# Kernel optimization log

Hardware: AMD Instinct MI355X
Metric: run time of the kernel (lower is better)

The kernel has to match this reference:

```python
import jax, jax.numpy as jnp
import numpy as np

D_MODEL = 1024
N_HEADS = 16
D_HEAD = D_MODEL // N_HEADS


def setup_inputs() -> dict:
    key = jax.random.key(0)
    ks = jax.random.split(key, 11)
    s = 0.02
    return {
        "X": jax.random.normal(ks[0], (4, 2048, D_MODEL), dtype=jnp.float32),
        "ln_gamma": jnp.ones((D_MODEL,), jnp.float32),
        "ln_beta": jnp.zeros((D_MODEL,), jnp.float32),
        "Wq": jax.random.normal(ks[1], (D_MODEL, D_MODEL), jnp.float32) * s,
        "bq": jnp.zeros((D_MODEL,), jnp.float32),
        "Wk": jax.random.normal(ks[2], (D_MODEL, D_MODEL), jnp.float32) * s,
        "bk": jnp.zeros((D_MODEL,), jnp.float32),
        "Wv": jax.random.normal(ks[3], (D_MODEL, D_MODEL), jnp.float32) * s,
        "bv": jnp.zeros((D_MODEL,), jnp.float32),
        "Wo": jax.random.normal(ks[4], (D_MODEL, D_MODEL), jnp.float32) * s,
        "bo": jnp.zeros((D_MODEL,), jnp.float32),
    }


def _attention(X, ln_gamma, ln_beta, Wq, bq, Wk, bk, Wv, bv, Wo, bo):
    B, S, D = X.shape
    H, Dh = N_HEADS, D_HEAD
    # LayerNorm over last dim
    mu = jnp.mean(X, axis=-1, keepdims=True)
    var = jnp.mean(jnp.square(X - mu), axis=-1, keepdims=True)
    Xn = (X - mu) * jax.lax.rsqrt(var + 1e-5) * ln_gamma + ln_beta
    # Projections (torch Linear: x @ W.T + b; W is [out, in])
    Q = (Xn @ Wq.T + bq).reshape(B, S, H, Dh).transpose(0, 2, 1, 3)
    K = (Xn @ Wk.T + bk).reshape(B, S, H, Dh).transpose(0, 2, 1, 3)
    V = (Xn @ Wv.T + bv).reshape(B, S, H, Dh).transpose(0, 2, 1, 3)
    scale = 1.0 / np.sqrt(Dh).astype(np.float32)
    scores = jnp.einsum("bhqd,bhkd->bhqk", Q * scale, K)  # [B,H,S,S]
    # p_dropout = 0.0 -> dropout is identity (applied before mask in original)
    # additive causal mask: 0 where q >= k, -inf otherwise
    causal = jnp.tril(jnp.ones((S, S), jnp.bool_))
    scores = jnp.where(causal, scores, -jnp.inf)
    A = jax.nn.softmax(scores, axis=-1)
    AV = jnp.einsum("bhqk,bhkd->bhqd", A, V)
    merged = AV.transpose(0, 2, 1, 3).reshape(B, S, D)
    return merged @ Wo.T + bo


def reference(X, ln_gamma, ln_beta, Wq, bq, Wk, bk, Wv, bv, Wo, bo):
    return _attention(X, ln_gamma, ln_beta, Wq, bq, Wk, bk, Wv, bv, Wo, bo)
```

## Files before the change

kernel.cpp:

```cpp
#include <hip/hip_runtime.h>

#define D_MODEL 1024
#define N_HEADS 16
#define D_HEAD 64
#define BATCH 4
#define SEQ 2048
#define TOKENS (BATCH * SEQ)
#define D_QKV 3072

#define QBLK 64
#define KBLK 64

typedef __attribute__((ext_vector_type(8))) short short8;
typedef __attribute__((ext_vector_type(4))) float f32x4;

__device__ __forceinline__ unsigned short f2bf(float f) {
    unsigned u = __float_as_uint(f);
    u += 0x7fffu + ((u >> 16) & 1u);
    return (unsigned short)(u >> 16);
}
__device__ __forceinline__ void gload16(const unsigned short* g, unsigned short* lds) {
    __builtin_amdgcn_global_load_lds((const __attribute__((address_space(1))) void*)g,
                                     (__attribute__((address_space(3))) void*)lds, 16, 0, 0);
}

__global__ void ln_kernel(const float* __restrict__ X, const float* __restrict__ gamma,
                          const float* __restrict__ beta, unsigned short* __restrict__ Xn) {
    const int t = blockIdx.x;
    const int tid = threadIdx.x;
    const float4 v = ((const float4*)(X + (size_t)t * D_MODEL))[tid];
    float s  = v.x + v.y + v.z + v.w;
    float s2 = v.x * v.x + v.y * v.y + v.z * v.z + v.w * v.w;
    for (int off = 32; off > 0; off >>= 1) {
        s  += __shfl_xor(s,  off);
        s2 += __shfl_xor(s2, off);
    }
    __shared__ float sh[8];
    const int wv = tid >> 6;
    if ((tid & 63) == 0) { sh[wv] = s; sh[4 + wv] = s2; }
    __syncthreads();
    const float ts  = sh[0] + sh[1] + sh[2] + sh[3];
    const float ts2 = sh[4] + sh[5] + sh[6] + sh[7];
    const float mu  = ts * (1.0f / D_MODEL);
    const float var = ts2 * (1.0f / D_MODEL) - mu * mu;
    const float rs  = rsqrtf(var + 1e-5f);
    const float4 gm = ((const float4*)gamma)[tid];
    const float4 bt = ((const float4*)beta)[tid];
    ushort4 o;
    o.x = f2bf((v.x - mu) * rs * gm.x + bt.x);
    o.y = f2bf((v.y - mu) * rs * gm.y + bt.y);
    o.z = f2bf((v.z - mu) * rs * gm.z + bt.z);
    o.w = f2bf((v.w - mu) * rs * gm.w + bt.w);
    ((ushort4*)Xn)[(size_t)t * (D_MODEL / 4) + tid] = o;
}

__global__ void cvt_all(const float* __restrict__ Wq, const float* __restrict__ Wk,
                        const float* __restrict__ Wv, const float* __restrict__ Wo,
                        unsigned short* __restrict__ Wqkv, unsigned short* __restrict__ WoB) {
    const int i = blockIdx.x * blockDim.x + threadIdx.x;
    const int mtx  = i >> 18;
    const int elem = i & 262143;
    const float* src;
    unsigned short* dst;
    if (mtx == 0)      { src = Wq; dst = Wqkv; }
    else if (mtx == 1) { src = Wk; dst = Wqkv + (1 << 20); }
    else if (mtx == 2) { src = Wv; dst = Wqkv + (2 << 20); }
    else               { src = Wo; dst = WoB; }
    const float4 v = ((const float4*)src)[elem];
    ushort4 o;
    o.x = f2bf(v.x); o.y = f2bf(v.y); o.z = f2bf(v.z); o.w = f2bf(v.w);
    ((ushort4*)dst)[elem] = o;
}

__global__ void transpose_v(const unsigned short* __restrict__ QKV, unsigned short* __restrict__ out) {
    __shared__ __attribute__((aligned(16))) unsigned short T[64][72];
    const int tid = threadIdx.x;
    const int s0 = blockIdx.x * 64;
    const int n0 = blockIdx.y * 64;
    const int b  = blockIdx.z;
    const int r = tid >> 2, c = (tid & 3) * 16;
    const unsigned short* ip = QKV + ((size_t)(b * SEQ + s0 + r)) * D_QKV + 2048 + n0 + c;
    *(short8*)&T[r][c]     = *(const short8*)ip;
    *(short8*)&T[r][c + 8] = *(const short8*)(ip + 8);
    __syncthreads();
    unsigned short* op = out + ((size_t)(b * D_MODEL + n0 + r)) * SEQ + s0 + c;
    short8 o0, o1;
    #pragma unroll
    for (int j = 0; j < 8; ++j) { o0[j] = (short)T[c + j][r]; o1[j] = (short)T[c + 8 + j][r]; }
    *(short8*)op       = o0;
    *(short8*)(op + 8) = o1;
}

template <bool OUT_BF16>
__global__ __launch_bounds__(256) void gemm128(const unsigned short* __restrict__ A,
                                               const unsigned short* __restrict__ B,
                                               const float* __restrict__ b0,
                                               const float* __restrict__ b1,
                                               const float* __restrict__ b2,
                                               void* __restrict__ out,
                                               int M, int N, int K, float qscale) {
    __shared__ __attribute__((aligned(16))) unsigned short As[2][128 * 64];
    __shared__ __attribute__((aligned(16))) unsigned short Bs[2][128 * 64];
    const int tid  = threadIdx.x;
    const int lane = tid & 63;
    const int w    = tid >> 6;
    const int wm = w >> 1, wn = w & 1;
    const int m0 = blockIdx.y * 128;
    const int n0 = blockIdx.x * 128;
    const int lr = lane & 15, lg = lane >> 4;

    const int crow  = lane >> 3;
    const int uslot = (lane & 7) ^ crow;

    const unsigned short* Ab = A + (size_t)m0 * K + uslot * 8;
    const unsigned short* Bb = B + (size_t)n0 * K + uslot * 8;

    #pragma unroll
    for (int i = 0; i < 4; ++i) {
        const int c = w * 4 + i;
        const int grow = c * 8 + crow;
        gload16(Ab + (size_t)grow * K, &As[0][c * 512]);
        gload16(Bb + (size_t)grow * K, &Bs[0][c * 512]);
    }
    __syncthreads();

    f32x4 acc[4][4] = {};
    const int NT = K >> 6;
    int cur = 0;
    for (int kt = 0; kt < NT; ++kt) {
        if (kt + 1 < NT) {
            const int k1 = (kt + 1) << 6;
            #pragma unroll
            for (int i = 0; i < 4; ++i) {
                const int c = w * 4 + i;
                const int grow = c * 8 + crow;
                gload16(Ab + (size_t)grow * K + k1, &As[cur ^ 1][c * 512]);
                gload16(Bb + (size_t)grow * K + k1, &Bs[cur ^ 1][c * 512]);
            }
        }
        #pragma unroll
        for (int h = 0; h < 2; ++h) {
            short8 af[4], bf[4];
            #pragma unroll
            for (int mi = 0; mi < 4; ++mi) {
                const int row = wm * 64 + mi * 16 + lr;
                const int slot = (h * 4 + lg) ^ (row & 7);
                af[mi] = *(const short8*)(&As[cur][row * 64 + slot * 8]);
            }
            #pragma unroll
            for (int ni = 0; ni < 4; ++ni) {
                const int row = wn * 64 + ni * 16 + lr;
                const int slot = (h * 4 + lg) ^ (row & 7);
                bf[ni] = *(const short8*)(&Bs[cur][row * 64 + slot * 8]);
            }
            #pragma unroll
            for (int mi = 0; mi < 4; ++mi)
                #pragma unroll
                for (int ni = 0; ni < 4; ++ni)
                    acc[mi][ni] = __builtin_amdgcn_mfma_f32_16x16x32_bf16(af[mi], bf[ni], acc[mi][ni], 0, 0, 0);
        }
        __syncthreads();
        cur ^= 1;
    }

    const int seg = blockIdx.x >> 3;
    const float* bp = (seg == 0) ? b0 : (seg == 1) ? b1 : b2;
    const float osc = (seg == 0) ? qscale : 1.0f;
    #pragma unroll
    for (int ni = 0; ni < 4; ++ni) {
        const int n = n0 + wn * 64 + ni * 16 + lr;
        const float bv = bp[n & 1023];
        #pragma unroll
        for (int mi = 0; mi < 4; ++mi) {
            const int mb = m0 + wm * 64 + mi * 16 + lg * 4;
            #pragma unroll
            for (int i = 0; i < 4; ++i) {
                const float val = (acc[mi][ni][i] + bv) * osc;
                if (OUT_BF16) ((unsigned short*)out)[(size_t)(mb + i) * N + n] = f2bf(val);
                else          ((float*)out)[(size_t)(mb + i) * N + n] = val;
            }
        }
    }
}

__global__ __launch_bounds__(256) void flash_attn(const unsigned short* __restrict__ QKV,
                                                  const unsigned short* __restrict__ Vt,
                                                  unsigned short* __restrict__ Mo) {
    __shared__ __attribute__((aligned(16))) unsigned short KtL[2][KBLK * 64];
    __shared__ __attribute__((aligned(16))) unsigned short VsL[2][64 * KBLK];
    __shared__ __attribute__((aligned(16))) unsigned int   Pq[4 * 16 * 32];

    const int tid  = threadIdx.x;
    const int lane = tid & 63;
    const int w    = tid >> 6;
    const int F   = blockIdx.x;
    const int xcd = F & 7;
    const int r_  = F >> 3;
    const int qb  = 31 - (r_ & 31);
    const int bh  = xcd | ((r_ >> 5) << 3);
    const int b = bh >> 4, h = bh & 15;
    const int q0 = qb * QBLK;
    const int lg = lane >> 4;
    const int lr = lane & 15;

    const size_t tokbase = (size_t)b * SEQ;
    const size_t hoff = (size_t)h * D_HEAD;

    const int crow  = lane >> 3;
    const int uslot = (lane & 7) ^ crow;

    const short* Qp = (const short*)QKV + (tokbase + q0 + w * 16 + lr) * D_QKV + hoff + lg * 8;
    const short8 qf0 = *(const short8*)(Qp);
    const short8 qf1 = *(const short8*)(Qp + 32);

    const unsigned short* Kg = QKV + (tokbase) * D_QKV + 1024 + hoff + uslot * 8;
    const unsigned short* Vg = Vt + ((size_t)bh * 64) * SEQ + uslot * 8;

    int koff[2][4];
    #pragma unroll
    for (int hh = 0; hh < 2; ++hh)
        #pragma unroll
        for (int s4 = 0; s4 < 4; ++s4)
            koff[hh][s4] = (s4 * 16 + lr) * 64 + (((hh * 4 + lg) ^ (lr & 7)) * 8);

    const int sxor = lr & 3;
    const int pw   = w * 512 + lr * 32 + lg * 2;
    int prd[2];
    #pragma unroll
    for (int c2 = 0; c2 < 2; ++c2)
        prd[c2] = w * 512 + lr * 32 + (lg & 1) * 4 + ((((c2 << 1) + (lg >> 1)) ^ sxor) << 3);

    int qaddr[4];
    #pragma unroll
    for (int i = 0; i < 4; ++i) qaddr[i] = (lg * 4 + i) * 4;

    float m = -INFINITY, l = 0.f;
    f32x4 acc[4] = {};

    const int ntiles = qb + 1;

    #pragma unroll
    for (int i = 0; i < 2; ++i) {
        const int c = w * 2 + i;
        const int row = c * 8 + crow;
        gload16(Kg + (size_t)row * D_QKV, &KtL[0][c * 512]);
        gload16(Vg + (size_t)row * SEQ, &VsL[0][c * 512]);
    }
    __syncthreads();

    int cur = 0;
    for (int t = 0; t < ntiles; ++t) {
        if (t + 1 < ntiles) {
            const int k1 = (t + 1) * KBLK;
            #pragma unroll
            for (int i = 0; i < 2; ++i) {
                const int c = w * 2 + i;
                const int row = c * 8 + crow;
                gload16(Kg + (size_t)(k1 + row) * D_QKV, &KtL[cur ^ 1][c * 512]);
                gload16(Vg + (size_t)row * SEQ + k1, &VsL[cur ^ 1][c * 512]);
            }
        }
        const unsigned short* Kc = KtL[cur];
        const unsigned short* Vc = VsL[cur];

        f32x4 st[4];
        __builtin_amdgcn_s_setprio(1);
        #pragma unroll
        for (int s4 = 0; s4 < 4; ++s4) {
            const short8 kf0 = *(const short8*)(Kc + koff[0][s4]);
            const short8 kf1 = *(const short8*)(Kc + koff[1][s4]);
            f32x4 z = {0.f, 0.f, 0.f, 0.f};
            z = __builtin_amdgcn_mfma_f32_16x16x32_bf16(kf0, qf0, z, 0, 0, 0);
            z = __builtin_amdgcn_mfma_f32_16x16x32_bf16(kf1, qf1, z, 0, 0, 0);
            st[s4] = z;
        }
        __builtin_amdgcn_s_setprio(0);

        if (t == qb) {
            const int qloc = w * 16 + lr;
            #pragma unroll
            for (int s4 = 0; s4 < 4; ++s4) {
                const int kb = s4 * 16 + lg * 4;
                #pragma unroll
                for (int r = 0; r < 4; ++r)
                    st[s4][r] = (kb + r <= qloc) ? st[s4][r] : -INFINITY;
            }
        }

        float pmax = st[0][0];
        #pragma unroll
        for (int s4 = 0; s4 < 4; ++s4)
            #pragma unroll
            for (int r = 0; r < 4; ++r) pmax = fmaxf(pmax, st[s4][r]);
        pmax = fmaxf(pmax, __shfl_xor(pmax, 16));
        pmax = fmaxf(pmax, __shfl_xor(pmax, 32));

        if (__any(pmax > m + 8.0f)) {
            const float mn = fmaxf(m, pmax);
            const float c  = __builtin_exp2f(m - mn);
            m = mn;
            l *= c;
            #pragma unroll
            for (int i = 0; i < 4; ++i) {
                const float cb = __uint_as_float(
                    (unsigned)__builtin_amdgcn_ds_bpermute(qaddr[i], (int)__float_as_uint(c)));
                #pragma unroll
                for (int ds = 0; ds < 4; ++ds) acc[ds][i] *= cb;
            }
        }

        float rs = 0.f;
        #pragma unroll
        for (int s4 = 0; s4 < 4; ++s4) {
            float p0 = __builtin_exp2f(st[s4][0] - m);
            float p1 = __builtin_exp2f(st[s4][1] - m);
            float p2 = __builtin_exp2f(st[s4][2] - m);
            float p3 = __builtin_exp2f(st[s4][3] - m);
            rs += (p0 + p1) + (p2 + p3);
            const unsigned u0 = __float_as_uint(p0) + 0x8000u;
            const unsigned u1 = __float_as_uint(p1) + 0x8000u;
            const unsigned u2 = __float_as_uint(p2) + 0x8000u;
            const unsigned u3 = __float_as_uint(p3) + 0x8000u;
            const int pb = pw + (((s4 ^ sxor) << 3));
            Pq[pb]     = (u1 & 0xffff0000u) | (u0 >> 16);
            Pq[pb + 1] = (u3 & 0xffff0000u) | (u2 >> 16);
        }
        rs += __shfl_xor(rs, 16);
        rs += __shfl_xor(rs, 32);
        l += rs;

        __builtin_amdgcn_s_setprio(1);
        #pragma unroll
        for (int c2 = 0; c2 < 2; ++c2) {
            const short8 pf = *(const short8*)(Pq + prd[c2]);
            #pragma unroll
            for (int ds = 0; ds < 4; ++ds) {
                const short8 vf = *(const short8*)(Vc + koff[c2][ds]);
                acc[ds] = __builtin_amdgcn_mfma_f32_16x16x32_bf16(pf, vf, acc[ds], 0, 0, 0);
            }
        }
        __builtin_amdgcn_s_setprio(0);

        __syncthreads();
        cur ^= 1;
    }

    const float linv = 1.0f / l;
    float lb[4];
    #pragma unroll
    for (int i = 0; i < 4; ++i)
        lb[i] = __uint_as_float(
            (unsigned)__builtin_amdgcn_ds_bpermute(qaddr[i], (int)__float_as_uint(linv)));
    const int gq = q0 + w * 16 + lg * 4;
    #pragma unroll
    for (int ds = 0; ds < 4; ++ds) {
        #pragma unroll
        for (int i = 0; i < 4; ++i) {
            const float o = acc[ds][i] * lb[i];
            Mo[(tokbase + gq + i) * D_MODEL + hoff + ds * 16 + lr] = f2bf(o);
        }
    }
}

extern "C" void kernel_launch(void* const* d_in, const int* in_sizes, int n_in,
                              void* d_out, int out_size, void* d_ws, size_t ws_size,
                              hipStream_t stream) {
    const float* X  = (const float*)d_in[0];
    const float* lg = (const float*)d_in[1];
    const float* lb = (const float*)d_in[2];
    const float* Wq = (const float*)d_in[3];
    const float* bq = (const float*)d_in[4];
    const float* Wk = (const float*)d_in[5];
    const float* bk = (const float*)d_in[6];
    const float* Wv = (const float*)d_in[7];
    const float* bv = (const float*)d_in[8];
    const float* Wo = (const float*)d_in[9];
    const float* bo = (const float*)d_in[10];
    float* out = (float*)d_out;

    char* ws = (char*)d_ws;
    const size_t MB = 1024 * 1024;
    unsigned short* Xn   = (unsigned short*)(ws + 0);
    unsigned short* Vtg  = (unsigned short*)(ws + 0);
    unsigned short* Wqkv = (unsigned short*)(ws + 16 * MB);
    unsigned short* WoB  = (unsigned short*)(ws + 22 * MB);
    unsigned short* QKVb = (unsigned short*)(ws + 24 * MB);
    unsigned short* Mb   = (unsigned short*)(ws + 72 * MB);

    ln_kernel<<<TOKENS, 256, 0, stream>>>(X, lg, lb, Xn);

    cvt_all<<<4096, 256, 0, stream>>>(Wq, Wk, Wv, Wo, Wqkv, WoB);

    const float qscale = 0.125f * 1.44269504088896f;
    dim3 qkvgrid(D_QKV / 128, TOKENS / 128);
    gemm128<true><<<qkvgrid, 256, 0, stream>>>(Xn, Wqkv, bq, bk, bv, QKVb,
                                               TOKENS, D_QKV, D_MODEL, qscale);

    dim3 tgrid(SEQ / 64, D_MODEL / 64, BATCH);
    transpose_v<<<tgrid, 256, 0, stream>>>(QKVb, Vtg);

    flash_attn<<<(SEQ / QBLK) * BATCH * N_HEADS, 256, 0, stream>>>(QKVb, Vtg, Mb);

    dim3 ogrid(D_MODEL / 128, TOKENS / 128);
    gemm128<false><<<ogrid, 256, 0, stream>>>(Mb, WoB, bo, bo, bo, out,
                                              TOKENS, D_MODEL, D_MODEL, 1.0f);
}
```

Measured before the change: 310.8 us.

## Fuse V transpose into QKV GEMM epilogue and keep P in registers

The QKV GEMM epilogue now writes V directly in transposed layout to a separate buffer and packs Q/K with a 2048 stride, which removes the standalone transpose kernel and its round trip through memory. Flash attention drops the LDS staging of P: probabilities stay in registers and feed a 16x16x16 bf16 MFMA with operands swapped, producing the output transposed, so the row-scale bpermutes go away and the output store becomes vectorized. The trade-off is narrower MFMAs (more instructions), narrower V fragment LDS reads, and scattered 8-byte stores of transposed V in the GEMM epilogue.

```diff
diff --git a/kernel.cpp b/kernel.cpp
--- a/kernel.cpp
+++ b/kernel.cpp
@@ -7,11 +7,14 @@
 #define SEQ 2048
 #define TOKENS (BATCH * SEQ)
 #define D_QKV 3072
+#define QKSTR 2048
 
 #define QBLK 64
 #define KBLK 64
 
 typedef __attribute__((ext_vector_type(8))) short short8;
+typedef __attribute__((ext_vector_type(4))) short short4v;
+typedef __attribute__((ext_vector_type(4))) unsigned short us4;
 typedef __attribute__((ext_vector_type(4))) float f32x4;
 
 __device__ __forceinline__ unsigned short f2bf(float f) {
@@ -72,32 +75,14 @@
     ((ushort4*)dst)[elem] = o;
 }
 
-__global__ void transpose_v(const unsigned short* __restrict__ QKV, unsigned short* __restrict__ out) {
-    __shared__ __attribute__((aligned(16))) unsigned short T[64][72];
-    const int tid = threadIdx.x;
-    const int s0 = blockIdx.x * 64;
-    const int n0 = blockIdx.y * 64;
-    const int b  = blockIdx.z;
-    const int r = tid >> 2, c = (tid & 3) * 16;
-    const unsigned short* ip = QKV + ((size_t)(b * SEQ + s0 + r)) * D_QKV + 2048 + n0 + c;
-    *(short8*)&T[r][c]     = *(const short8*)ip;
-    *(short8*)&T[r][c + 8] = *(const short8*)(ip + 8);
-    __syncthreads();
-    unsigned short* op = out + ((size_t)(b * D_MODEL + n0 + r)) * SEQ + s0 + c;
-    short8 o0, o1;
-    #pragma unroll
-    for (int j = 0; j < 8; ++j) { o0[j] = (short)T[c + j][r]; o1[j] = (short)T[c + 8 + j][r]; }
-    *(short8*)op       = o0;
-    *(short8*)(op + 8) = o1;
-}
-
-template <bool OUT_BF16>
+template <int MODE>
 __global__ __launch_bounds__(256) void gemm128(const unsigned short* __restrict__ A,
                                                const unsigned short* __restrict__ B,
                                                const float* __restrict__ b0,
                                                const float* __restrict__ b1,
                                                const float* __restrict__ b2,
                                                void* __restrict__ out,
+                                               unsigned short* __restrict__ vtout,
                                                int M, int N, int K, float qscale) {
     __shared__ __attribute__((aligned(16))) unsigned short As[2][128 * 64];
     __shared__ __attribute__((aligned(16))) unsigned short Bs[2][128 * 64];
@@ -166,29 +151,46 @@
     const int seg = blockIdx.x >> 3;
     const float* bp = (seg == 0) ? b0 : (seg == 1) ? b1 : b2;
     const float osc = (seg == 0) ? qscale : 1.0f;
-    #pragma unroll
-    for (int ni = 0; ni < 4; ++ni) {
-        const int n = n0 + wn * 64 + ni * 16 + lr;
-        const float bv = bp[n & 1023];
-        #pragma unroll
-        for (int mi = 0; mi < 4; ++mi) {
-            const int mb = m0 + wm * 64 + mi * 16 + lg * 4;
-            #pragma unroll
-            for (int i = 0; i < 4; ++i) {
-                const float val = (acc[mi][ni][i] + bv) * osc;
-                if (OUT_BF16) ((unsigned short*)out)[(size_t)(mb + i) * N + n] = f2bf(val);
-                else          ((float*)out)[(size_t)(mb + i) * N + n] = val;
-            }
-        }
-    }
-}
-
-__global__ __launch_bounds__(256) void flash_attn(const unsigned short* __restrict__ QKV,
+    if (MODE == 2 && seg == 2) {
+        #pragma unroll
+        for (int ni = 0; ni < 4; ++ni) {
+            const int np = n0 + wn * 64 + ni * 16 + lr - 2048;
+            const float bv = bp[np];
+            #pragma unroll
+            for (int mi = 0; mi < 4; ++mi) {
+                const int mb = m0 + wm * 64 + mi * 16 + lg * 4;
+                const int bb = mb >> 11;
+                const int sm = mb & 2047;
+                us4 o;
+                #pragma unroll
+                for (int i = 0; i < 4; ++i) o[i] = f2bf(acc[mi][ni][i] + bv);
+                *(us4*)(vtout + (size_t)(bb * 1024 + np) * SEQ + sm) = o;
+            }
+        }
+    } else {
+        #pragma unroll
+        for (int ni = 0; ni < 4; ++ni) {
+            const int n = n0 + wn * 64 + ni * 16 + lr;
+            const float bv = bp[n & 1023];
+            #pragma unroll
+            for (int mi = 0; mi < 4; ++mi) {
+                const int mb = m0 + wm * 64 + mi * 16 + lg * 4;
+                #pragma unroll
+                for (int i = 0; i < 4; ++i) {
+                    const float val = (acc[mi][ni][i] + bv) * osc;
+                    if (MODE == 0) ((float*)out)[(size_t)(mb + i) * N + n] = val;
+                    else           ((unsigned short*)out)[(size_t)(mb + i) * QKSTR + n] = f2bf(val);
+                }
+            }
+        }
+    }
+}
+
+__global__ __launch_bounds__(256) void flash_attn(const unsigned short* __restrict__ QK,
                                                   const unsigned short* __restrict__ Vt,
                                                   unsigned short* __restrict__ Mo) {
     __shared__ __attribute__((aligned(16))) unsigned short KtL[2][KBLK * 64];
     __shared__ __attribute__((aligned(16))) unsigned short VsL[2][64 * KBLK];
-    __shared__ __attribute__((aligned(16))) unsigned int   Pq[4 * 16 * 32];
 
     const int tid  = threadIdx.x;
     const int lane = tid & 63;
@@ -209,12 +211,16 @@
     const int crow  = lane >> 3;
     const int uslot = (lane & 7) ^ crow;
 
-    const short* Qp = (const short*)QKV + (tokbase + q0 + w * 16 + lr) * D_QKV + hoff + lg * 8;
+    const short* Qp = (const short*)QK + (tokbase + q0 + w * 16 + lr) * QKSTR + hoff + lg * 8;
     const short8 qf0 = *(const short8*)(Qp);
     const short8 qf1 = *(const short8*)(Qp + 32);
 
-    const unsigned short* Kg = QKV + (tokbase) * D_QKV + 1024 + hoff + uslot * 8;
-    const unsigned short* Vg = Vt + ((size_t)bh * 64) * SEQ + uslot * 8;
+    const unsigned short* kld[2];
+    const unsigned short* vld[2];
+    kld[0] = QK + (tokbase + w * 16 + crow) * QKSTR + 1024 + hoff + uslot * 8;
+    kld[1] = kld[0] + (size_t)8 * QKSTR;
+    vld[0] = Vt + ((size_t)bh * 64 + w * 16 + crow) * SEQ + uslot * 8;
+    vld[1] = vld[0] + (size_t)8 * SEQ;
 
     int koff[2][4];
     #pragma unroll
@@ -222,42 +228,33 @@
         #pragma unroll
         for (int s4 = 0; s4 < 4; ++s4)
             koff[hh][s4] = (s4 * 16 + lr) * 64 + (((hh * 4 + lg) ^ (lr & 7)) * 8);
-
-    const int sxor = lr & 3;
-    const int pw   = w * 512 + lr * 32 + lg * 2;
-    int prd[2];
+    int voff[4][4];
     #pragma unroll
-    for (int c2 = 0; c2 < 2; ++c2)
-        prd[c2] = w * 512 + lr * 32 + (lg & 1) * 4 + ((((c2 << 1) + (lg >> 1)) ^ sxor) << 3);
-
-    int qaddr[4];
-    #pragma unroll
-    for (int i = 0; i < 4; ++i) qaddr[i] = (lg * 4 + i) * 4;
+    for (int ds = 0; ds < 4; ++ds)
+        #pragma unroll
+        for (int s4 = 0; s4 < 4; ++s4)
+            voff[ds][s4] = (ds * 16 + lr) * 64 + (((s4 * 2 + (lg >> 1)) ^ (lr & 7)) << 3) + ((lg & 1) << 2);
 
     float m = -INFINITY, l = 0.f;
     f32x4 acc[4] = {};
 
     const int ntiles = qb + 1;
 
-    #pragma unroll
-    for (int i = 0; i < 2; ++i) {
-        const int c = w * 2 + i;
-        const int row = c * 8 + crow;
-        gload16(Kg + (size_t)row * D_QKV, &KtL[0][c * 512]);
-        gload16(Vg + (size_t)row * SEQ, &VsL[0][c * 512]);
-    }
+    gload16(kld[0], &KtL[0][(w * 2) * 512]);
+    gload16(kld[1], &KtL[0][(w * 2 + 1) * 512]);
+    gload16(vld[0], &VsL[0][(w * 2) * 512]);
+    gload16(vld[1], &VsL[0][(w * 2 + 1) * 512]);
     __syncthreads();
 
     int cur = 0;
     for (int t = 0; t < ntiles; ++t) {
         if (t + 1 < ntiles) {
-            const int k1 = (t + 1) * KBLK;
             #pragma unroll
             for (int i = 0; i < 2; ++i) {
-                const int c = w * 2 + i;
-                const int row = c * 8 + crow;
-                gload16(Kg + (size_t)(k1 + row) * D_QKV, &KtL[cur ^ 1][c * 512]);
-                gload16(Vg + (size_t)row * SEQ + k1, &VsL[cur ^ 1][c * 512]);
+                kld[i] += (size_t)KBLK * QKSTR;
+                vld[i] += KBLK;
+                gload16(kld[i], &KtL[cur ^ 1][(w * 2 + i) * 512]);
+                gload16(vld[i], &VsL[cur ^ 1][(w * 2 + i) * 512]);
             }
         }
         const unsigned short* Kc = KtL[cur];
@@ -301,29 +298,20 @@
             m = mn;
             l *= c;
             #pragma unroll
-            for (int i = 0; i < 4; ++i) {
-                const float cb = __uint_as_float(
-                    (unsigned)__builtin_amdgcn_ds_bpermute(qaddr[i], (int)__float_as_uint(c)));
-                #pragma unroll
-                for (int ds = 0; ds < 4; ++ds) acc[ds][i] *= cb;
-            }
+            for (int ds = 0; ds < 4; ++ds)
+                #pragma unroll
+                for (int i = 0; i < 4; ++i) acc[ds][i] *= c;
         }
 
         float rs = 0.f;
         #pragma unroll
         for (int s4 = 0; s4 < 4; ++s4) {
-            float p0 = __builtin_exp2f(st[s4][0] - m);
-            float p1 = __builtin_exp2f(st[s4][1] - m);
-            float p2 = __builtin_exp2f(st[s4][2] - m);
-            float p3 = __builtin_exp2f(st[s4][3] - m);
-            rs += (p0 + p1) + (p2 + p3);
-            const unsigned u0 = __float_as_uint(p0) + 0x8000u;
-            const unsigned u1 = __float_as_uint(p1) + 0x8000u;
-            const unsigned u2 = __float_as_uint(p2) + 0x8000u;
-            const unsigned u3 = __float_as_uint(p3) + 0x8000u;
-            const int pb = pw + (((s4 ^ sxor) << 3));
-            Pq[pb]     = (u1 & 0xffff0000u) | (u0 >> 16);
-            Pq[pb + 1] = (u3 & 0xffff0000u) | (u2 >> 16);
+            #pragma unroll
+            for (int r = 0; r < 4; ++r) {
+                const float p = __builtin_exp2f(st[s4][r] - m);
+                st[s4][r] = p;
+                rs += p;
+            }
         }
         rs += __shfl_xor(rs, 16);
         rs += __shfl_xor(rs, 32);
@@ -331,12 +319,15 @@
 
         __builtin_amdgcn_s_setprio(1);
         #pragma unroll
-        for (int c2 = 0; c2 < 2; ++c2) {
-            const short8 pf = *(const short8*)(Pq + prd[c2]);
+        for (int s4 = 0; s4 < 4; ++s4) {
+            short4v pf;
+            #pragma unroll
+            for (int r = 0; r < 4; ++r)
+                pf[r] = (short)((__float_as_uint(st[s4][r]) + 0x8000u) >> 16);
             #pragma unroll
             for (int ds = 0; ds < 4; ++ds) {
-                const short8 vf = *(const short8*)(Vc + koff[c2][ds]);
-                acc[ds] = __builtin_amdgcn_mfma_f32_16x16x32_bf16(pf, vf, acc[ds], 0, 0, 0);
+                const short4v vf = *(const short4v*)(Vc + voff[ds][s4]);
+                acc[ds] = __builtin_amdgcn_mfma_f32_16x16x16bf16_1k(vf, pf, acc[ds], 0, 0, 0);
             }
         }
         __builtin_amdgcn_s_setprio(0);
@@ -346,19 +337,13 @@
     }
 
     const float linv = 1.0f / l;
-    float lb[4];
-    #pragma unroll
-    for (int i = 0; i < 4; ++i)
-        lb[i] = __uint_as_float(
-            (unsigned)__builtin_amdgcn_ds_bpermute(qaddr[i], (int)__float_as_uint(linv)));
-    const int gq = q0 + w * 16 + lg * 4;
+    const size_t obase = (tokbase + q0 + w * 16 + lr) * D_MODEL + hoff + lg * 4;
     #pragma unroll
     for (int ds = 0; ds < 4; ++ds) {
-        #pragma unroll
-        for (int i = 0; i < 4; ++i) {
-            const float o = acc[ds][i] * lb[i];
-            Mo[(tokbase + gq + i) * D_MODEL + hoff + ds * 16 + lr] = f2bf(o);
-        }
+        us4 o;
+        #pragma unroll
+        for (int i = 0; i < 4; ++i) o[i] = f2bf(acc[ds][i] * linv);
+        *(us4*)(Mo + obase + ds * 16) = o;
     }
 }
 
@@ -381,10 +366,10 @@
     char* ws = (char*)d_ws;
     const size_t MB = 1024 * 1024;
     unsigned short* Xn   = (unsigned short*)(ws + 0);
-    unsigned short* Vtg  = (unsigned short*)(ws + 0);
     unsigned short* Wqkv = (unsigned short*)(ws + 16 * MB);
     unsigned short* WoB  = (unsigned short*)(ws + 22 * MB);
-    unsigned short* QKVb = (unsigned short*)(ws + 24 * MB);
+    unsigned short* QKb  = (unsigned short*)(ws + 24 * MB);
+    unsigned short* Vtg  = (unsigned short*)(ws + 56 * MB);
     unsigned short* Mb   = (unsigned short*)(ws + 72 * MB);
 
     ln_kernel<<<TOKENS, 256, 0, stream>>>(X, lg, lb, Xn);
@@ -393,15 +378,12 @@
 
     const float qscale = 0.125f * 1.44269504088896f;
     dim3 qkvgrid(D_QKV / 128, TOKENS / 128);
-    gemm128<true><<<qkvgrid, 256, 0, stream>>>(Xn, Wqkv, bq, bk, bv, QKVb,
-                                               TOKENS, D_QKV, D_MODEL, qscale);
-
-    dim3 tgrid(SEQ / 64, D_MODEL / 64, BATCH);
-    transpose_v<<<tgrid, 256, 0, stream>>>(QKVb, Vtg);
-
-    flash_attn<<<(SEQ / QBLK) * BATCH * N_HEADS, 256, 0, stream>>>(QKVb, Vtg, Mb);
+    gemm128<2><<<qkvgrid, 256, 0, stream>>>(Xn, Wqkv, bq, bk, bv, QKb, Vtg,
+                                            TOKENS, D_QKV, D_MODEL, qscale);
+
+    flash_attn<<<(SEQ / QBLK) * BATCH * N_HEADS, 256, 0, stream>>>(QKb, Vtg, Mb);
 
     dim3 ogrid(D_MODEL / 128, TOKENS / 128);
-    gemm128<false><<<ogrid, 256, 0, stream>>>(Mb, WoB, bo, bo, bo, out,
-                                              TOKENS, D_MODEL, D_MODEL, 1.0f);
-}
+    gemm128<0><<<ogrid, 256, 0, stream>>>(Mb, WoB, bo, bo, bo, out, nullptr,
+                                          TOKENS, D_MODEL, D_MODEL, 1.0f);
+}
```

After: 303.7 us. 2.3% less time.
